# Optimization experiments

Measured on AMD Instinct MI355X. Metric: run time of the kernel, lower is better.

## Reference

```python
import jax, jax.numpy as jnp
import numpy as np

B, S, D = 2, 2048, 1024
H = 16
HD = D // H
SCALE = float(np.sqrt(HD))


def setup_inputs() -> dict:
    key = jax.random.key(0)
    ks = jax.random.split(key, 10)
    def lin(k):
        # xavier_uniform for [out, in] = [D, D]
        bound = float(np.sqrt(6.0 / (D + D)))
        return jax.random.uniform(k, (D, D), jnp.float32, -bound, bound)
    return {
        "hidden_states": jax.random.normal(ks[0], (B, S, D), jnp.float32),
        "attention_mask": jnp.ones((B, S), jnp.float32),
        "Wq": lin(ks[1]), "bq": jnp.zeros((D,), jnp.float32),
        "Wk": lin(ks[2]), "bk": jnp.zeros((D,), jnp.float32),
        "Wv": lin(ks[3]), "bv": jnp.zeros((D,), jnp.float32),
        "Wo": lin(ks[4]), "bo": jnp.zeros((D,), jnp.float32),
    }


def _heads(x):
    # [B,S,D] -> [B,H,S,HD]
    return x.reshape(B, S, H, HD).transpose(0, 2, 1, 3)


def secure_softmax(scores):
    c = jnp.clip(scores, -3.0, 3.0)
    sig = 0.5 + 0.25 * c - 0.01 * c ** 3
    sig = jnp.clip(sig, 0.01, 0.99)
    return sig / (jnp.sum(sig, axis=-1, keepdims=True) + 1e-8)


def reference(hidden_states, attention_mask, Wq, bq, Wk, bk, Wv, bv, Wo, bo):
    q = _heads(hidden_states @ Wq.T + bq)
    k = _heads(hidden_states @ Wk.T + bk)
    v = _heads(hidden_states @ Wv.T + bv)
    # [B,H,S,S]
    scores = jnp.einsum("bhqd,bhkd->bhqk", q, k) / SCALE
    scores = scores + (1.0 - attention_mask[:, None, None, :]) * -10000.0
    probs = secure_softmax(scores)
    ctx = jnp.einsum("bhqk,bhkd->bhqd", probs, v)
    ctx = ctx.transpose(0, 2, 1, 3).reshape(B, S, D)
    return ctx @ Wo.T + bo
```

## Files before the change

kernel.cpp:

```cpp
#include <hip/hip_runtime.h>
#include <stdint.h>

#define B_ 2
#define S_ 2048
#define D_ 1024
#define H_ 16
#define HD_ 64
#define M_ (B_*S_)

typedef __bf16 bf16;
typedef __attribute__((ext_vector_type(8))) __bf16 bf16x8;
typedef __attribute__((ext_vector_type(4))) float f32x4;

__device__ __forceinline__ void gload16(const bf16* g, bf16* l) {
    __builtin_amdgcn_global_load_lds(
        (const __attribute__((address_space(1))) void*)g,
        (__attribute__((address_space(3))) void*)l, 16, 0, 0);
}

__global__ void k_cvt_all(const float* __restrict__ hs,
                          const float* __restrict__ Wq, const float* __restrict__ Wk,
                          const float* __restrict__ Wv, const float* __restrict__ Wo,
                          bf16* __restrict__ hb,
                          bf16* __restrict__ wqb, bf16* __restrict__ wkb,
                          bf16* __restrict__ wvb, bf16* __restrict__ wob) {
    int blk = blockIdx.x;
    const float* s; bf16* d; int base;
    if (blk < 2048) { s = hs; d = hb; base = blk; }
    else {
        int r = blk - 2048; int which = r >> 9; base = r & 511;
        s = (which==0)?Wq:(which==1)?Wk:(which==2)?Wv:Wo;
        d = (which==0)?wqb:(which==1)?wkb:(which==2)?wvb:wob;
    }
    int idx = base*2048 + threadIdx.x*8;
    float4 a = *(const float4*)(s + idx);
    float4 b = *(const float4*)(s + idx + 4);
    bf16 o[8] = {(bf16)a.x,(bf16)a.y,(bf16)a.z,(bf16)a.w,
                 (bf16)b.x,(bf16)b.y,(bf16)b.z,(bf16)b.w};
    *(int4*)(d + idx) = *(const int4*)o;
}

__global__ __launch_bounds__(256) void k_gemm_qkv(
    const bf16* __restrict__ X,
    const bf16* __restrict__ Wq, const bf16* __restrict__ Wk, const bf16* __restrict__ Wv,
    const float* __restrict__ bq, const float* __restrict__ bk, const float* __restrict__ bv,
    bf16* __restrict__ Qo, bf16* __restrict__ Ko, bf16* __restrict__ Vo)
{
    const int z = blockIdx.z;
    const bf16* W = (z==0) ? Wq : (z==1) ? Wk : Wv;
    const float* bias = (z==0) ? bq : (z==1) ? bk : bv;
    const int n0 = blockIdx.x * 128;
    const int m0 = blockIdx.y * 128;
    const int t = threadIdx.x;
    const int w = t >> 6, lane = t & 63, quad = lane >> 4, l15 = lane & 15;
    const int lr = lane >> 3;
    const int lc = (lane & 7) ^ lr;
    const int sx = l15 & 7;
    const int mw = (w >> 1) * 64, nw = (w & 1) * 64;

    __shared__ __align__(16) char smraw[128*136*2];
    bf16* As  = (bf16*)smraw;
    bf16* Bs  = (bf16*)(smraw + 16384);
    bf16* epi = (bf16*)smraw;

    f32x4 acc[4][4];
    #pragma unroll
    for (int i = 0; i < 4; i++)
        #pragma unroll
        for (int j = 0; j < 4; j++)
            acc[i][j] = (f32x4){0.f,0.f,0.f,0.f};

    const bf16* gA = X + (size_t)(m0 + w*8 + lr)*D_ + lc*8;
    const bf16* gB = W + (size_t)(n0 + w*8 + lr)*D_ + lc*8;

    for (int k0 = 0; k0 < D_; k0 += 64) {
        #pragma unroll
        for (int c = 0; c < 4; c++) {
            gload16(gA + (size_t)c*32*D_ + k0, &As[c*2048 + w*512]);
            gload16(gB + (size_t)c*32*D_ + k0, &Bs[c*2048 + w*512]);
        }
        __syncthreads();
        #pragma unroll
        for (int ks = 0; ks < 2; ks++) {
            bf16x8 af[4], bfr[4];
            #pragma unroll
            for (int i = 0; i < 4; i++)
                af[i] = *(const bf16x8*)&As[(mw + i*16 + l15)*64 + (((ks*4+quad)^sx)*8)];
            #pragma unroll
            for (int j = 0; j < 4; j++)
                bfr[j] = *(const bf16x8*)&Bs[(nw + j*16 + l15)*64 + (((ks*4+quad)^sx)*8)];
            #pragma unroll
            for (int i = 0; i < 4; i++)
                #pragma unroll
                for (int j = 0; j < 4; j++)
                    acc[i][j] = __builtin_amdgcn_mfma_f32_16x16x32_bf16(af[i], bfr[j], acc[i][j], 0, 0, 0);
        }
        __syncthreads();
    }

    const float scale = (z == 0) ? 0.125f : 1.0f;
    if (z == 2) {
        #pragma unroll
        for (int j = 0; j < 4; j++) {
            int n = nw + j*16 + l15;
            float bn = bias[n0 + n];
            #pragma unroll
            for (int i = 0; i < 4; i++) {
                int mloc = mw + i*16 + quad*4;
                union { bf16 h4[4]; uint2 u; } pk;
                #pragma unroll
                for (int r = 0; r < 4; r++) pk.h4[r] = (bf16)(acc[i][j][r] + bn);
                *(uint2*)&epi[n*136 + mloc] = pk.u;
            }
        }
    } else {
        #pragma unroll
        for (int j = 0; j < 4; j++) {
            int n = nw + j*16 + l15;
            float bn = bias[n0 + n];
            #pragma unroll
            for (int i = 0; i < 4; i++) {
                int mloc = mw + i*16 + quad*4;
                #pragma unroll
                for (int r = 0; r < 4; r++)
                    epi[(mloc + r)*136 + n] = (bf16)((acc[i][j][r] + bn) * scale);
            }
        }
    }
    __syncthreads();
    if (z == 2) {
        #pragma unroll
        for (int kk = 0; kk < 8; kk++) {
            int c = t + 256*kk;
            int row = c >> 4;
            int mcol = (c & 15) * 8;
            int4 val = *(const int4*)&epi[row*136 + mcol];
            int n = n0 + row; int hh = n >> 6, hd = n & 63;
            int m = m0 + mcol; int bb = m >> 11, s = m & 2047;
            *(int4*)&Vo[((size_t)((bb*H_ + hh)*HD_ + hd))*S_ + s] = val;
        }
    } else {
        bf16* Out = (z == 0) ? Qo : Ko;
        #pragma unroll
        for (int kk = 0; kk < 8; kk++) {
            int c = t + 256*kk;
            int row = c >> 4;
            int ncol = (c & 15) * 8;
            int4 val = *(const int4*)&epi[row*136 + ncol];
            int m = m0 + row; int bb = m >> 11, s = m & 2047;
            int n = n0 + ncol; int hh = n >> 6, hd = n & 63;
            *(int4*)&Out[((size_t)((bb*H_ + hh)*S_ + s))*HD_ + hd] = val;
        }
    }
}

__global__ __launch_bounds__(256) void k_gemm_out(
    const bf16* __restrict__ X, const bf16* __restrict__ W,
    const float* __restrict__ bias, float* __restrict__ Out)
{
    const int n0 = blockIdx.x * 128;
    const int m0 = blockIdx.y * 64;
    const int t = threadIdx.x;
    const int w = t >> 6, lane = t & 63, quad = lane >> 4, l15 = lane & 15;
    const int lr = lane >> 3;
    const int lc = (lane & 7) ^ lr;
    const int sx = l15 & 7;
    const int nw = w * 32;

    __shared__ __align__(16) bf16 As[64*64];
    __shared__ __align__(16) bf16 Bs[128*64];

    f32x4 acc[4][2];
    #pragma unroll
    for (int i = 0; i < 4; i++)
        #pragma unroll
        for (int j = 0; j < 2; j++)
            acc[i][j] = (f32x4){0.f,0.f,0.f,0.f};

    const bf16* gA = X + (size_t)(m0 + w*8 + lr)*D_ + lc*8;
    const bf16* gB = W + (size_t)(n0 + w*8 + lr)*D_ + lc*8;

    for (int k0 = 0; k0 < D_; k0 += 64) {
        #pragma unroll
        for (int c = 0; c < 2; c++)
            gload16(gA + (size_t)c*32*D_ + k0, &As[c*2048 + w*512]);
        #pragma unroll
        for (int c = 0; c < 4; c++)
            gload16(gB + (size_t)c*32*D_ + k0, &Bs[c*2048 + w*512]);
        __syncthreads();
        #pragma unroll
        for (int ks = 0; ks < 2; ks++) {
            bf16x8 af[4], bfr[2];
            #pragma unroll
            for (int i = 0; i < 4; i++)
                af[i] = *(const bf16x8*)&As[(i*16 + l15)*64 + (((ks*4+quad)^sx)*8)];
            #pragma unroll
            for (int j = 0; j < 2; j++)
                bfr[j] = *(const bf16x8*)&Bs[(nw + j*16 + l15)*64 + (((ks*4+quad)^sx)*8)];
            #pragma unroll
            for (int i = 0; i < 4; i++)
                #pragma unroll
                for (int j = 0; j < 2; j++)
                    acc[i][j] = __builtin_amdgcn_mfma_f32_16x16x32_bf16(af[i], bfr[j], acc[i][j], 0, 0, 0);
        }
        __syncthreads();
    }

    #pragma unroll
    for (int j = 0; j < 2; j++) {
        int n = n0 + nw + j*16 + l15;
        float bn = bias[n];
        #pragma unroll
        for (int i = 0; i < 4; i++) {
            int mbase = m0 + i*16 + quad*4;
            #pragma unroll
            for (int r = 0; r < 4; r++)
                Out[(size_t)(mbase + r)*D_ + n] = acc[i][j][r] + bn;
        }
    }
}

__global__ __launch_bounds__(256, 2) void k_attn(
    const bf16* __restrict__ Q, const bf16* __restrict__ K, const bf16* __restrict__ Vt,
    const float* __restrict__ mask, bf16* __restrict__ Ctx)
{
    const int bh = blockIdx.y;
    const int b = bh >> 4, h = bh & 15;
    const int q0 = blockIdx.x * 128;
    const int t = threadIdx.x;
    const int w = t >> 6, lane = t & 63, quad = lane >> 4, l15 = lane & 15;
    const int lr = lane >> 3;
    const int lc = (lane & 7) ^ lr;
    const int sx = l15 & 7;

    __shared__ __align__(16) bf16 Ks[2][64*64];
    __shared__ __align__(16) bf16 Vs[2][64*64];
    __shared__ __align__(16) bf16 Ps[128*64];
    __shared__ float lsumP[4][128];

    bf16x8 qf[8][2];
    const bf16* Qbase = Q + ((size_t)bh*S_ + q0)*HD_;
    #pragma unroll
    for (int qs = 0; qs < 8; qs++)
        #pragma unroll
        for (int ks = 0; ks < 2; ks++)
            qf[qs][ks] = *(const bf16x8*)&Qbase[(size_t)(qs*16 + l15)*HD_ + ks*32 + quad*8];

    f32x4 cacc[2][4];
    #pragma unroll
    for (int i = 0; i < 2; i++)
        #pragma unroll
        for (int j = 0; j < 4; j++)
            cacc[i][j] = (f32x4){0.f,0.f,0.f,0.f};
    float lac[8];
    #pragma unroll
    for (int qs = 0; qs < 8; qs++) lac[qs] = 0.f;

    const bf16* Kst = K + ((size_t)bh*S_ + w*8 + lr)*HD_ + lc*8;
    const bf16* Vst = Vt + ((size_t)bh*HD_ + w*8 + lr)*S_ + lc*8;

    #pragma unroll
    for (int c = 0; c < 2; c++)
        gload16(Kst + (size_t)c*32*HD_, &Ks[0][c*2048 + w*512]);
    #pragma unroll
    for (int c = 0; c < 2; c++)
        gload16(Vst + (size_t)c*32*S_, &Vs[0][c*2048 + w*512]);
    __syncthreads();

    for (int it = 0; it < S_/64; it++) {
        const int cur = it & 1;
        const int k0 = it*64;

        f32x4 st[8];
        #pragma unroll
        for (int qs = 0; qs < 8; qs++) st[qs] = (f32x4){0.f,0.f,0.f,0.f};
        #pragma unroll
        for (int ks = 0; ks < 2; ks++) {
            bf16x8 af = *(const bf16x8*)&Ks[cur][(w*16 + l15)*64 + (((ks*4+quad)^sx)*8)];
            #pragma unroll
            for (int qs = 0; qs < 8; qs++)
                st[qs] = __builtin_amdgcn_mfma_f32_16x16x32_bf16(af, qf[qs][ks], st[qs], 0, 0, 0);
        }

        float4 m4 = *(const float4*)&mask[(size_t)b*S_ + k0 + w*16 + quad*4];
        float mv[4] = {(1.0f-m4.x)*-10000.0f, (1.0f-m4.y)*-10000.0f,
                       (1.0f-m4.z)*-10000.0f, (1.0f-m4.w)*-10000.0f};
        const int c8 = (w*2 + (quad>>1)) ^ sx;
        #pragma unroll
        for (int qs = 0; qs < 8; qs++) {
            union { bf16 h4[4]; uint2 u; } pk;
            #pragma unroll
            for (int r = 0; r < 4; r++) {
                float s = st[qs][r] + mv[r];
                float c = __builtin_amdgcn_fmed3f(s, -3.0f, 3.0f);
                float u = fmaf(c*c, -0.01f, 0.25f);
                float sg = fmaf(c, u, 0.5f);
                sg = __builtin_amdgcn_fmed3f(sg, 0.01f, 0.99f);
                lac[qs] += sg;
                pk.h4[r] = (bf16)sg;
            }
            *(uint2*)&Ps[(qs*16 + l15)*64 + c8*8 + (quad&1)*4] = pk.u;
        }
        __syncthreads();

        if (it < S_/64 - 1) {
            const int nxt = cur ^ 1, k1 = k0 + 64;
            #pragma unroll
            for (int c = 0; c < 2; c++)
                gload16(Kst + (size_t)(k1 + c*32)*HD_, &Ks[nxt][c*2048 + w*512]);
            #pragma unroll
            for (int c = 0; c < 2; c++)
                gload16(Vst + (size_t)c*32*S_ + k1, &Vs[nxt][c*2048 + w*512]);
        }

        #pragma unroll
        for (int ks = 0; ks < 2; ks++) {
            bf16x8 pf[2], vf[4];
            #pragma unroll
            for (int m2 = 0; m2 < 2; m2++)
                pf[m2] = *(const bf16x8*)&Ps[(w*32 + m2*16 + l15)*64 + (((ks*4+quad)^sx)*8)];
            #pragma unroll
            for (int nt = 0; nt < 4; nt++)
                vf[nt] = *(const bf16x8*)&Vs[cur][(nt*16 + l15)*64 + (((ks*4+quad)^sx)*8)];
            #pragma unroll
            for (int m2 = 0; m2 < 2; m2++)
                #pragma unroll
                for (int nt = 0; nt < 4; nt++)
                    cacc[m2][nt] = __builtin_amdgcn_mfma_f32_16x16x32_bf16(pf[m2], vf[nt], cacc[m2][nt], 0, 0, 0);
        }
        __syncthreads();
    }

    #pragma unroll
    for (int qs = 0; qs < 8; qs++) {
        float v = lac[qs];
        v += __shfl_xor(v, 16);
        v += __shfl_xor(v, 32);
        if (quad == 0) lsumP[w][qs*16 + l15] = v;
    }
    __syncthreads();

    #pragma unroll
    for (int m2 = 0; m2 < 2; m2++) {
        #pragma unroll
        for (int r = 0; r < 4; r++) {
            int q = w*32 + m2*16 + quad*4 + r;
            float s = lsumP[0][q] + lsumP[1][q] + lsumP[2][q] + lsumP[3][q];
            float rinv = 1.0f / (s + 1e-8f);
            size_t row = (size_t)(b*S_ + q0 + q);
            #pragma unroll
            for (int nt = 0; nt < 4; nt++)
                Ctx[row*D_ + h*HD_ + nt*16 + l15] = (bf16)(cacc[m2][nt][r] * rinv);
        }
    }
}

extern "C" void kernel_launch(void* const* d_in, const int* in_sizes, int n_in,
                              void* d_out, int out_size, void* d_ws, size_t ws_size,
                              hipStream_t stream) {
    const float* hs   = (const float*)d_in[0];
    const float* mask = (const float*)d_in[1];
    const float* Wq   = (const float*)d_in[2];
    const float* bq   = (const float*)d_in[3];
    const float* Wk   = (const float*)d_in[4];
    const float* bk   = (const float*)d_in[5];
    const float* Wv   = (const float*)d_in[6];
    const float* bv   = (const float*)d_in[7];
    const float* Wo   = (const float*)d_in[8];
    const float* bo   = (const float*)d_in[9];
    float* out = (float*)d_out;

    char* ws = (char*)d_ws;
    const size_t MB = 1024*1024;
    bf16* hb   = (bf16*)(ws);
    bf16* wqb  = (bf16*)(ws + 8*MB);
    bf16* wkb  = (bf16*)(ws + 10*MB);
    bf16* wvb  = (bf16*)(ws + 12*MB);
    bf16* wob  = (bf16*)(ws + 14*MB);
    bf16* qb   = (bf16*)(ws + 16*MB);
    bf16* kb   = (bf16*)(ws + 24*MB);
    bf16* vtb  = (bf16*)(ws + 32*MB);
    bf16* ctxb = (bf16*)(ws + 40*MB);

    k_cvt_all<<<2048 + 4*512, 256, 0, stream>>>(hs, Wq, Wk, Wv, Wo, hb, wqb, wkb, wvb, wob);

    k_gemm_qkv<<<dim3(D_/128, M_/128, 3), 256, 0, stream>>>(
        hb, wqb, wkb, wvb, bq, bk, bv, qb, kb, vtb);

    k_attn<<<dim3(S_/128, B_*H_), 256, 0, stream>>>(qb, kb, vtb, mask, ctxb);

    k_gemm_out<<<dim3(D_/128, M_/64), 256, 0, stream>>>(ctxb, wob, bo, out);
}
```

Before: 209.4 us.

## Restructure attention so each wave owns 32 queries with register-streamed K/V

The attention kernel now gives each wave its own 32 query rows. Each wave loads K and V fragments directly from global memory into registers, prefetching the next tile, instead of staging them cooperatively through double-buffered LDS. The probability tile is kept in a per-wave LDS buffer, which removes the block-wide barriers and the cross-wave row-sum reduction. The polynomial sigmoid is written with packed 2-wide float vectors. The trade-off is that each wave now re-reads K and V from global memory or cache (four times the traffic per block) and uses more registers.

```diff
diff --git a/kernel.cpp b/kernel.cpp
--- a/kernel.cpp
+++ b/kernel.cpp
@@ -11,6 +11,7 @@
 typedef __bf16 bf16;
 typedef __attribute__((ext_vector_type(8))) __bf16 bf16x8;
 typedef __attribute__((ext_vector_type(4))) float f32x4;
+typedef __attribute__((ext_vector_type(2))) float f32x2;
 
 __device__ __forceinline__ void gload16(const bf16* g, bf16* l) {
     __builtin_amdgcn_global_load_lds(
@@ -226,25 +227,26 @@
 {
     const int bh = blockIdx.y;
     const int b = bh >> 4, h = bh & 15;
-    const int q0 = blockIdx.x * 128;
     const int t = threadIdx.x;
     const int w = t >> 6, lane = t & 63, quad = lane >> 4, l15 = lane & 15;
-    const int lr = lane >> 3;
-    const int lc = (lane & 7) ^ lr;
-    const int sx = l15 & 7;
-
-    __shared__ __align__(16) bf16 Ks[2][64*64];
-    __shared__ __align__(16) bf16 Vs[2][64*64];
-    __shared__ __align__(16) bf16 Ps[128*64];
-    __shared__ float lsumP[4][128];
-
-    bf16x8 qf[8][2];
-    const bf16* Qbase = Q + ((size_t)bh*S_ + q0)*HD_;
-    #pragma unroll
-    for (int qs = 0; qs < 8; qs++)
-        #pragma unroll
-        for (int ks = 0; ks < 2; ks++)
-            qf[qs][ks] = *(const bf16x8*)&Qbase[(size_t)(qs*16 + l15)*HD_ + ks*32 + quad*8];
+    const int q0 = blockIdx.x * 128 + w * 32;
+    const int s7 = l15 & 7;
+
+    __shared__ __align__(16) bf16 Pw[4][32*64];
+    __shared__ float lsw[4][32];
+
+    bf16x8 qf[2][2];
+    {
+        const bf16* Qb = Q + ((size_t)bh*S_ + q0)*HD_;
+        #pragma unroll
+        for (int nt = 0; nt < 2; nt++)
+            #pragma unroll
+            for (int ks = 0; ks < 2; ks++)
+                qf[nt][ks] = *(const bf16x8*)&Qb[(size_t)(nt*16 + l15)*HD_ + ks*32 + quad*8];
+    }
+
+    const bf16* Kb = K + (size_t)bh*S_*HD_ + (size_t)l15*HD_ + quad*8;
+    const bf16* Vb = Vt + (size_t)bh*HD_*S_ + (size_t)l15*S_ + quad*8;
 
     f32x4 cacc[2][4];
     #pragma unroll
@@ -252,105 +254,120 @@
         #pragma unroll
         for (int j = 0; j < 4; j++)
             cacc[i][j] = (f32x4){0.f,0.f,0.f,0.f};
-    float lac[8];
-    #pragma unroll
-    for (int qs = 0; qs < 8; qs++) lac[qs] = 0.f;
-
-    const bf16* Kst = K + ((size_t)bh*S_ + w*8 + lr)*HD_ + lc*8;
-    const bf16* Vst = Vt + ((size_t)bh*HD_ + w*8 + lr)*S_ + lc*8;
-
-    #pragma unroll
-    for (int c = 0; c < 2; c++)
-        gload16(Kst + (size_t)c*32*HD_, &Ks[0][c*2048 + w*512]);
-    #pragma unroll
-    for (int c = 0; c < 2; c++)
-        gload16(Vst + (size_t)c*32*S_, &Vs[0][c*2048 + w*512]);
-    __syncthreads();
+    f32x2 lac[2] = {(f32x2){0.f,0.f}, (f32x2){0.f,0.f}};
+
+    bf16x8 ka[4][2], vb[4][2];
+    #pragma unroll
+    for (int mt = 0; mt < 4; mt++)
+        #pragma unroll
+        for (int ks = 0; ks < 2; ks++)
+            ka[mt][ks] = *(const bf16x8*)&Kb[(size_t)(mt*16)*HD_ + ks*32];
+    #pragma unroll
+    for (int nt2 = 0; nt2 < 4; nt2++)
+        #pragma unroll
+        for (int ch = 0; ch < 2; ch++)
+            vb[nt2][ch] = *(const bf16x8*)&Vb[(size_t)(nt2*16)*S_ + ch*32];
 
     for (int it = 0; it < S_/64; it++) {
-        const int cur = it & 1;
         const int k0 = it*64;
 
-        f32x4 st[8];
-        #pragma unroll
-        for (int qs = 0; qs < 8; qs++) st[qs] = (f32x4){0.f,0.f,0.f,0.f};
-        #pragma unroll
-        for (int ks = 0; ks < 2; ks++) {
-            bf16x8 af = *(const bf16x8*)&Ks[cur][(w*16 + l15)*64 + (((ks*4+quad)^sx)*8)];
-            #pragma unroll
-            for (int qs = 0; qs < 8; qs++)
-                st[qs] = __builtin_amdgcn_mfma_f32_16x16x32_bf16(af, qf[qs][ks], st[qs], 0, 0, 0);
-        }
-
-        float4 m4 = *(const float4*)&mask[(size_t)b*S_ + k0 + w*16 + quad*4];
-        float mv[4] = {(1.0f-m4.x)*-10000.0f, (1.0f-m4.y)*-10000.0f,
-                       (1.0f-m4.z)*-10000.0f, (1.0f-m4.w)*-10000.0f};
-        const int c8 = (w*2 + (quad>>1)) ^ sx;
-        #pragma unroll
-        for (int qs = 0; qs < 8; qs++) {
-            union { bf16 h4[4]; uint2 u; } pk;
-            #pragma unroll
-            for (int r = 0; r < 4; r++) {
-                float s = st[qs][r] + mv[r];
-                float c = __builtin_amdgcn_fmed3f(s, -3.0f, 3.0f);
-                float u = fmaf(c*c, -0.01f, 0.25f);
-                float sg = fmaf(c, u, 0.5f);
-                sg = __builtin_amdgcn_fmed3f(sg, 0.01f, 0.99f);
-                lac[qs] += sg;
-                pk.h4[r] = (bf16)sg;
+        float4 mk[4];
+        #pragma unroll
+        for (int mt = 0; mt < 4; mt++)
+            mk[mt] = *(const float4*)&mask[(size_t)b*S_ + k0 + mt*16 + quad*4];
+
+        f32x4 st[4][2];
+        #pragma unroll
+        for (int mt = 0; mt < 4; mt++)
+            #pragma unroll
+            for (int nt = 0; nt < 2; nt++)
+                st[mt][nt] = (f32x4){0.f,0.f,0.f,0.f};
+        #pragma unroll
+        for (int ks = 0; ks < 2; ks++)
+            #pragma unroll
+            for (int mt = 0; mt < 4; mt++)
+                #pragma unroll
+                for (int nt = 0; nt < 2; nt++)
+                    st[mt][nt] = __builtin_amdgcn_mfma_f32_16x16x32_bf16(ka[mt][ks], qf[nt][ks], st[mt][nt], 0, 0, 0);
+
+        if (it < S_/64 - 1) {
+            #pragma unroll
+            for (int mt = 0; mt < 4; mt++)
+                #pragma unroll
+                for (int ks = 0; ks < 2; ks++)
+                    ka[mt][ks] = *(const bf16x8*)&Kb[(size_t)(k0 + 64 + mt*16)*HD_ + ks*32];
+        }
+
+        #pragma unroll
+        for (int mt = 0; mt < 4; mt++) {
+            f32x2 mlo = {(1.0f - mk[mt].x)*-10000.0f, (1.0f - mk[mt].y)*-10000.0f};
+            f32x2 mhi = {(1.0f - mk[mt].z)*-10000.0f, (1.0f - mk[mt].w)*-10000.0f};
+            #pragma unroll
+            for (int nt = 0; nt < 2; nt++) {
+                f32x2 s0 = {st[mt][nt][0], st[mt][nt][1]};
+                f32x2 s1 = {st[mt][nt][2], st[mt][nt][3]};
+                s0 += mlo; s1 += mhi;
+                s0 = __builtin_elementwise_min(__builtin_elementwise_max(s0, (f32x2)(-3.0f)), (f32x2)(3.0f));
+                s1 = __builtin_elementwise_min(__builtin_elementwise_max(s1, (f32x2)(-3.0f)), (f32x2)(3.0f));
+                f32x2 g0 = s0 * (s0*s0*(f32x2)(-0.01f) + (f32x2)(0.25f)) + (f32x2)(0.5f);
+                f32x2 g1 = s1 * (s1*s1*(f32x2)(-0.01f) + (f32x2)(0.25f)) + (f32x2)(0.5f);
+                g0 = __builtin_elementwise_min(__builtin_elementwise_max(g0, (f32x2)(0.01f)), (f32x2)(0.99f));
+                g1 = __builtin_elementwise_min(__builtin_elementwise_max(g1, (f32x2)(0.01f)), (f32x2)(0.99f));
+                lac[nt] += g0 + g1;
+                union { bf16 h2[2]; uint32_t u; } p0, p1;
+                p0.h2[0] = (bf16)g0.x; p0.h2[1] = (bf16)g0.y;
+                p1.h2[0] = (bf16)g1.x; p1.h2[1] = (bf16)g1.y;
+                uint2 pk = {p0.u, p1.u};
+                int ql = nt*16 + l15;
+                *(uint2*)&Pw[w][ql*64 + (((mt*2 + (quad>>1)) ^ s7)*8) + (quad&1)*4] = pk;
             }
-            *(uint2*)&Ps[(qs*16 + l15)*64 + c8*8 + (quad&1)*4] = pk.u;
-        }
-        __syncthreads();
+        }
+
+        bf16x8 pf[2][2];
+        #pragma unroll
+        for (int ch = 0; ch < 2; ch++)
+            #pragma unroll
+            for (int nt = 0; nt < 2; nt++)
+                pf[ch][nt] = *(const bf16x8*)&Pw[w][(nt*16 + l15)*64 + (((ch*4 + quad) ^ s7)*8)];
+
+        #pragma unroll
+        for (int ch = 0; ch < 2; ch++)
+            #pragma unroll
+            for (int nt = 0; nt < 2; nt++)
+                #pragma unroll
+                for (int nt2 = 0; nt2 < 4; nt2++)
+                    cacc[nt][nt2] = __builtin_amdgcn_mfma_f32_16x16x32_bf16(pf[ch][nt], vb[nt2][ch], cacc[nt][nt2], 0, 0, 0);
 
         if (it < S_/64 - 1) {
-            const int nxt = cur ^ 1, k1 = k0 + 64;
-            #pragma unroll
-            for (int c = 0; c < 2; c++)
-                gload16(Kst + (size_t)(k1 + c*32)*HD_, &Ks[nxt][c*2048 + w*512]);
-            #pragma unroll
-            for (int c = 0; c < 2; c++)
-                gload16(Vst + (size_t)c*32*S_ + k1, &Vs[nxt][c*2048 + w*512]);
-        }
-
-        #pragma unroll
-        for (int ks = 0; ks < 2; ks++) {
-            bf16x8 pf[2], vf[4];
-            #pragma unroll
-            for (int m2 = 0; m2 < 2; m2++)
-                pf[m2] = *(const bf16x8*)&Ps[(w*32 + m2*16 + l15)*64 + (((ks*4+quad)^sx)*8)];
-            #pragma unroll
-            for (int nt = 0; nt < 4; nt++)
-                vf[nt] = *(const bf16x8*)&Vs[cur][(nt*16 + l15)*64 + (((ks*4+quad)^sx)*8)];
-            #pragma unroll
-            for (int m2 = 0; m2 < 2; m2++)
-                #pragma unroll
-                for (int nt = 0; nt < 4; nt++)
-                    cacc[m2][nt] = __builtin_amdgcn_mfma_f32_16x16x32_bf16(pf[m2], vf[nt], cacc[m2][nt], 0, 0, 0);
-        }
-        __syncthreads();
-    }
-
-    #pragma unroll
-    for (int qs = 0; qs < 8; qs++) {
-        float v = lac[qs];
+            #pragma unroll
+            for (int nt2 = 0; nt2 < 4; nt2++)
+                #pragma unroll
+                for (int ch = 0; ch < 2; ch++)
+                    vb[nt2][ch] = *(const bf16x8*)&Vb[(size_t)(nt2*16)*S_ + k0 + 64 + ch*32];
+        }
+    }
+
+    #pragma unroll
+    for (int nt = 0; nt < 2; nt++) {
+        float v = lac[nt].x + lac[nt].y;
         v += __shfl_xor(v, 16);
         v += __shfl_xor(v, 32);
-        if (quad == 0) lsumP[w][qs*16 + l15] = v;
-    }
-    __syncthreads();
-
-    #pragma unroll
-    for (int m2 = 0; m2 < 2; m2++) {
+        if (quad == 0) lsw[w][nt*16 + l15] = v;
+    }
+    f32x4 s4[2];
+    #pragma unroll
+    for (int nt = 0; nt < 2; nt++)
+        s4[nt] = *(const f32x4*)&lsw[w][nt*16 + quad*4];
+
+    #pragma unroll
+    for (int nt = 0; nt < 2; nt++) {
         #pragma unroll
         for (int r = 0; r < 4; r++) {
-            int q = w*32 + m2*16 + quad*4 + r;
-            float s = lsumP[0][q] + lsumP[1][q] + lsumP[2][q] + lsumP[3][q];
-            float rinv = 1.0f / (s + 1e-8f);
-            size_t row = (size_t)(b*S_ + q0 + q);
-            #pragma unroll
-            for (int nt = 0; nt < 4; nt++)
-                Ctx[row*D_ + h*HD_ + nt*16 + l15] = (bf16)(cacc[m2][nt][r] * rinv);
+            float rinv = 1.0f / (s4[nt][r] + 1e-8f);
+            size_t row = (size_t)(b*S_ + q0 + nt*16 + quad*4 + r);
+            #pragma unroll
+            for (int nt2 = 0; nt2 < 4; nt2++)
+                Ctx[row*D_ + h*HD_ + nt2*16 + l15] = (bf16)(cacc[nt][nt2][r] * rinv);
         }
     }
 }
```

Result: slower. 278.8 us (+33.1%).

## Split attention over key halves and fuse the partial combine into the output GEMM

Applied to the files above, without the earlier changes.

The attention kernel now launches a third grid dimension that splits the key sequence into two halves. Each half writes an unnormalized bf16 context and per-row sigmoid sums to separate workspace buffers, which reuse the memory of the dead hidden-state and Wq copies. The output projection GEMM loads both partials, adds them, divides by the summed normalizer, and writes the A tile to LDS through registers instead of the async global-to-LDS load. This doubles the number of attention blocks to fill more CUs, but adds extra partial-result traffic, a slower A-tile load path in the GEMM, and an extra bf16 rounding of the unnormalized partials.

```diff
diff --git a/kernel.cpp b/kernel.cpp
--- a/kernel.cpp
+++ b/kernel.cpp
@@ -155,7 +155,9 @@
 }
 
 __global__ __launch_bounds__(256) void k_gemm_out(
-    const bf16* __restrict__ X, const bf16* __restrict__ W,
+    const bf16* __restrict__ P0, const bf16* __restrict__ P1,
+    const float* __restrict__ L0, const float* __restrict__ L1,
+    const bf16* __restrict__ W,
     const float* __restrict__ bias, float* __restrict__ Out)
 {
     const int n0 = blockIdx.x * 128;
@@ -177,13 +179,26 @@
         for (int j = 0; j < 2; j++)
             acc[i][j] = (f32x4){0.f,0.f,0.f,0.f};
 
-    const bf16* gA = X + (size_t)(m0 + w*8 + lr)*D_ + lc*8;
     const bf16* gB = W + (size_t)(n0 + w*8 + lr)*D_ + lc*8;
 
     for (int k0 = 0; k0 < D_; k0 += 64) {
-        #pragma unroll
-        for (int c = 0; c < 2; c++)
-            gload16(gA + (size_t)c*32*D_ + k0, &As[c*2048 + w*512]);
+        const int head = k0 >> 6;
+        #pragma unroll
+        for (int c = 0; c < 2; c++) {
+            int row = m0 + c*32 + w*8 + lr;
+            int bb = row >> 11, s = row & 2047;
+            int lidx = (bb*H_ + head)*S_ + s;
+            float l = L0[lidx] + L1[lidx];
+            float inv = 1.0f / (l + 1e-8f);
+            size_t gofs = (size_t)row*D_ + k0 + lc*8;
+            bf16x8 a0 = *(const bf16x8*)&P0[gofs];
+            bf16x8 a1 = *(const bf16x8*)&P1[gofs];
+            bf16 o8[8];
+            #pragma unroll
+            for (int r = 0; r < 8; r++)
+                o8[r] = (bf16)(((float)a0[r] + (float)a1[r]) * inv);
+            *(int4*)&As[c*2048 + w*512 + lane*8] = *(const int4*)o8;
+        }
         #pragma unroll
         for (int c = 0; c < 4; c++)
             gload16(gB + (size_t)c*32*D_ + k0, &Bs[c*2048 + w*512]);
@@ -220,13 +235,18 @@
     }
 }
 
-__global__ __launch_bounds__(256, 2) void k_attn(
+__global__ __launch_bounds__(256) void k_attn(
     const bf16* __restrict__ Q, const bf16* __restrict__ K, const bf16* __restrict__ Vt,
-    const float* __restrict__ mask, bf16* __restrict__ Ctx)
+    const float* __restrict__ mask,
+    bf16* __restrict__ P0, bf16* __restrict__ P1,
+    float* __restrict__ L0, float* __restrict__ L1)
 {
     const int bh = blockIdx.y;
     const int b = bh >> 4, h = bh & 15;
     const int q0 = blockIdx.x * 128;
+    const int z = blockIdx.z;
+    bf16* __restrict__ Po = z ? P1 : P0;
+    float* __restrict__ Lo = z ? L1 : L0;
     const int t = threadIdx.x;
     const int w = t >> 6, lane = t & 63, quad = lane >> 4, l15 = lane & 15;
     const int lr = lane >> 3;
@@ -256,20 +276,21 @@
     #pragma unroll
     for (int qs = 0; qs < 8; qs++) lac[qs] = 0.f;
 
+    const int kb0 = z * (S_/2);
     const bf16* Kst = K + ((size_t)bh*S_ + w*8 + lr)*HD_ + lc*8;
     const bf16* Vst = Vt + ((size_t)bh*HD_ + w*8 + lr)*S_ + lc*8;
 
     #pragma unroll
     for (int c = 0; c < 2; c++)
-        gload16(Kst + (size_t)c*32*HD_, &Ks[0][c*2048 + w*512]);
+        gload16(Kst + (size_t)(kb0 + c*32)*HD_, &Ks[0][c*2048 + w*512]);
     #pragma unroll
     for (int c = 0; c < 2; c++)
-        gload16(Vst + (size_t)c*32*S_, &Vs[0][c*2048 + w*512]);
+        gload16(Vst + (size_t)c*32*S_ + kb0, &Vs[0][c*2048 + w*512]);
     __syncthreads();
 
-    for (int it = 0; it < S_/64; it++) {
+    for (int it = 0; it < S_/128; it++) {
         const int cur = it & 1;
-        const int k0 = it*64;
+        const int k0 = kb0 + it*64;
 
         f32x4 st[8];
         #pragma unroll
@@ -303,14 +324,14 @@
         }
         __syncthreads();
 
-        if (it < S_/64 - 1) {
-            const int nxt = cur ^ 1, k1 = k0 + 64;
+        if (it < S_/128 - 1) {
+            const int k1 = k0 + 64;
             #pragma unroll
             for (int c = 0; c < 2; c++)
-                gload16(Kst + (size_t)(k1 + c*32)*HD_, &Ks[nxt][c*2048 + w*512]);
+                gload16(Kst + (size_t)(k1 + c*32)*HD_, &Ks[cur^1][c*2048 + w*512]);
             #pragma unroll
             for (int c = 0; c < 2; c++)
-                gload16(Vst + (size_t)c*32*S_ + k1, &Vs[nxt][c*2048 + w*512]);
+                gload16(Vst + (size_t)c*32*S_ + k1, &Vs[cur^1][c*2048 + w*512]);
         }
 
         #pragma unroll
@@ -346,11 +367,12 @@
         for (int r = 0; r < 4; r++) {
             int q = w*32 + m2*16 + quad*4 + r;
             float s = lsumP[0][q] + lsumP[1][q] + lsumP[2][q] + lsumP[3][q];
-            float rinv = 1.0f / (s + 1e-8f);
+            if (l15 == 0)
+                Lo[(size_t)bh*S_ + q0 + q] = s;
             size_t row = (size_t)(b*S_ + q0 + q);
             #pragma unroll
             for (int nt = 0; nt < 4; nt++)
-                Ctx[row*D_ + h*HD_ + nt*16 + l15] = (bf16)(cacc[m2][nt][r] * rinv);
+                Po[row*D_ + h*HD_ + nt*16 + l15] = (bf16)cacc[m2][nt][r];
         }
     }
 }
@@ -372,22 +394,25 @@
 
     char* ws = (char*)d_ws;
     const size_t MB = 1024*1024;
-    bf16* hb   = (bf16*)(ws);
-    bf16* wqb  = (bf16*)(ws + 8*MB);
-    bf16* wkb  = (bf16*)(ws + 10*MB);
-    bf16* wvb  = (bf16*)(ws + 12*MB);
-    bf16* wob  = (bf16*)(ws + 14*MB);
-    bf16* qb   = (bf16*)(ws + 16*MB);
-    bf16* kb   = (bf16*)(ws + 24*MB);
-    bf16* vtb  = (bf16*)(ws + 32*MB);
-    bf16* ctxb = (bf16*)(ws + 40*MB);
+    bf16*  hb   = (bf16*)(ws);
+    bf16*  P1   = (bf16*)(ws);
+    bf16*  wqb  = (bf16*)(ws + 8*MB);
+    float* L0   = (float*)(ws + 8*MB);
+    float* L1   = (float*)(ws + 8*MB + 512*1024);
+    bf16*  wkb  = (bf16*)(ws + 10*MB);
+    bf16*  wvb  = (bf16*)(ws + 12*MB);
+    bf16*  wob  = (bf16*)(ws + 14*MB);
+    bf16*  qb   = (bf16*)(ws + 16*MB);
+    bf16*  kb   = (bf16*)(ws + 24*MB);
+    bf16*  vtb  = (bf16*)(ws + 32*MB);
+    bf16*  P0   = (bf16*)(ws + 40*MB);
 
     k_cvt_all<<<2048 + 4*512, 256, 0, stream>>>(hs, Wq, Wk, Wv, Wo, hb, wqb, wkb, wvb, wob);
 
     k_gemm_qkv<<<dim3(D_/128, M_/128, 3), 256, 0, stream>>>(
         hb, wqb, wkb, wvb, bq, bk, bv, qb, kb, vtb);
 
-    k_attn<<<dim3(S_/128, B_*H_), 256, 0, stream>>>(qb, kb, vtb, mask, ctxb);
-
-    k_gemm_out<<<dim3(D_/128, M_/64), 256, 0, stream>>>(ctxb, wob, bo, out);
-}
+    k_attn<<<dim3(S_/128, B_*H_, 2), 256, 0, stream>>>(qb, kb, vtb, mask, P0, P1, L0, L1);
+
+    k_gemm_out<<<dim3(D_/128, M_/64), 256, 0, stream>>>(P0, P1, L0, L1, wob, bo, out);
+}
```

After: 272.3 us. 30.1% more time.

## Halve attention query tile to 64 rows and single-buffer V with reordered prefetch

Applied to the files above, without the earlier changes.

The attention kernel now processes 64 query rows per block instead of 128, doubling the grid to 1024 blocks and roughly halving per-thread accumulator and Q-fragment registers. V shared memory goes from double to single buffering: V for the current tile is loaded at the top of each iteration, and the next K tile is prefetched alongside it. The launch-bounds occupancy hint is dropped. More blocks and less LDS should raise occupancy, but each K/V tile is now reloaded by twice as many blocks, and the V load is no longer overlapped with the previous iteration's compute.

```diff
diff --git a/kernel.cpp b/kernel.cpp
--- a/kernel.cpp
+++ b/kernel.cpp
@@ -220,13 +220,13 @@
     }
 }
 
-__global__ __launch_bounds__(256, 2) void k_attn(
+__global__ __launch_bounds__(256) void k_attn(
     const bf16* __restrict__ Q, const bf16* __restrict__ K, const bf16* __restrict__ Vt,
     const float* __restrict__ mask, bf16* __restrict__ Ctx)
 {
     const int bh = blockIdx.y;
     const int b = bh >> 4, h = bh & 15;
-    const int q0 = blockIdx.x * 128;
+    const int q0 = blockIdx.x * 64;
     const int t = threadIdx.x;
     const int w = t >> 6, lane = t & 63, quad = lane >> 4, l15 = lane & 15;
     const int lr = lane >> 3;
@@ -234,27 +234,24 @@
     const int sx = l15 & 7;
 
     __shared__ __align__(16) bf16 Ks[2][64*64];
-    __shared__ __align__(16) bf16 Vs[2][64*64];
-    __shared__ __align__(16) bf16 Ps[128*64];
-    __shared__ float lsumP[4][128];
-
-    bf16x8 qf[8][2];
+    __shared__ __align__(16) bf16 Vs[64*64];
+    __shared__ __align__(16) bf16 Ps[64*64];
+    __shared__ float lsumP[4][64];
+
+    bf16x8 qf[4][2];
     const bf16* Qbase = Q + ((size_t)bh*S_ + q0)*HD_;
     #pragma unroll
-    for (int qs = 0; qs < 8; qs++)
+    for (int qs = 0; qs < 4; qs++)
         #pragma unroll
         for (int ks = 0; ks < 2; ks++)
             qf[qs][ks] = *(const bf16x8*)&Qbase[(size_t)(qs*16 + l15)*HD_ + ks*32 + quad*8];
 
-    f32x4 cacc[2][4];
-    #pragma unroll
-    for (int i = 0; i < 2; i++)
-        #pragma unroll
-        for (int j = 0; j < 4; j++)
-            cacc[i][j] = (f32x4){0.f,0.f,0.f,0.f};
-    float lac[8];
-    #pragma unroll
-    for (int qs = 0; qs < 8; qs++) lac[qs] = 0.f;
+    f32x4 cacc[4];
+    #pragma unroll
+    for (int j = 0; j < 4; j++) cacc[j] = (f32x4){0.f,0.f,0.f,0.f};
+    float lac[4];
+    #pragma unroll
+    for (int qs = 0; qs < 4; qs++) lac[qs] = 0.f;
 
     const bf16* Kst = K + ((size_t)bh*S_ + w*8 + lr)*HD_ + lc*8;
     const bf16* Vst = Vt + ((size_t)bh*HD_ + w*8 + lr)*S_ + lc*8;
@@ -264,21 +261,32 @@
         gload16(Kst + (size_t)c*32*HD_, &Ks[0][c*2048 + w*512]);
     #pragma unroll
     for (int c = 0; c < 2; c++)
-        gload16(Vst + (size_t)c*32*S_, &Vs[0][c*2048 + w*512]);
+        gload16(Vst + (size_t)c*32*S_, &Vs[c*2048 + w*512]);
     __syncthreads();
 
     for (int it = 0; it < S_/64; it++) {
         const int cur = it & 1;
         const int k0 = it*64;
 
-        f32x4 st[8];
-        #pragma unroll
-        for (int qs = 0; qs < 8; qs++) st[qs] = (f32x4){0.f,0.f,0.f,0.f};
+        if (it > 0) {
+            #pragma unroll
+            for (int c = 0; c < 2; c++)
+                gload16(Vst + (size_t)c*32*S_ + k0, &Vs[c*2048 + w*512]);
+        }
+        if (it < S_/64 - 1) {
+            #pragma unroll
+            for (int c = 0; c < 2; c++)
+                gload16(Kst + (size_t)(k0 + 64 + c*32)*HD_, &Ks[cur^1][c*2048 + w*512]);
+        }
+
+        f32x4 st[4];
+        #pragma unroll
+        for (int qs = 0; qs < 4; qs++) st[qs] = (f32x4){0.f,0.f,0.f,0.f};
         #pragma unroll
         for (int ks = 0; ks < 2; ks++) {
             bf16x8 af = *(const bf16x8*)&Ks[cur][(w*16 + l15)*64 + (((ks*4+quad)^sx)*8)];
             #pragma unroll
-            for (int qs = 0; qs < 8; qs++)
+            for (int qs = 0; qs < 4; qs++)
                 st[qs] = __builtin_amdgcn_mfma_f32_16x16x32_bf16(af, qf[qs][ks], st[qs], 0, 0, 0);
         }
 
@@ -287,7 +295,7 @@
                        (1.0f-m4.z)*-10000.0f, (1.0f-m4.w)*-10000.0f};
         const int c8 = (w*2 + (quad>>1)) ^ sx;
         #pragma unroll
-        for (int qs = 0; qs < 8; qs++) {
+        for (int qs = 0; qs < 4; qs++) {
             union { bf16 h4[4]; uint2 u; } pk;
             #pragma unroll
             for (int r = 0; r < 4; r++) {
@@ -303,36 +311,22 @@
         }
         __syncthreads();
 
-        if (it < S_/64 - 1) {
-            const int nxt = cur ^ 1, k1 = k0 + 64;
-            #pragma unroll
-            for (int c = 0; c < 2; c++)
-                gload16(Kst + (size_t)(k1 + c*32)*HD_, &Ks[nxt][c*2048 + w*512]);
-            #pragma unroll
-            for (int c = 0; c < 2; c++)
-                gload16(Vst + (size_t)c*32*S_ + k1, &Vs[nxt][c*2048 + w*512]);
-        }
-
         #pragma unroll
         for (int ks = 0; ks < 2; ks++) {
-            bf16x8 pf[2], vf[4];
-            #pragma unroll
-            for (int m2 = 0; m2 < 2; m2++)
-                pf[m2] = *(const bf16x8*)&Ps[(w*32 + m2*16 + l15)*64 + (((ks*4+quad)^sx)*8)];
+            bf16x8 pf, vf[4];
+            pf = *(const bf16x8*)&Ps[(w*16 + l15)*64 + (((ks*4+quad)^sx)*8)];
             #pragma unroll
             for (int nt = 0; nt < 4; nt++)
-                vf[nt] = *(const bf16x8*)&Vs[cur][(nt*16 + l15)*64 + (((ks*4+quad)^sx)*8)];
-            #pragma unroll
-            for (int m2 = 0; m2 < 2; m2++)
-                #pragma unroll
-                for (int nt = 0; nt < 4; nt++)
-                    cacc[m2][nt] = __builtin_amdgcn_mfma_f32_16x16x32_bf16(pf[m2], vf[nt], cacc[m2][nt], 0, 0, 0);
-        }
-        __syncthreads();
-    }
-
-    #pragma unroll
-    for (int qs = 0; qs < 8; qs++) {
+                vf[nt] = *(const bf16x8*)&Vs[(nt*16 + l15)*64 + (((ks*4+quad)^sx)*8)];
+            #pragma unroll
+            for (int nt = 0; nt < 4; nt++)
+                cacc[nt] = __builtin_amdgcn_mfma_f32_16x16x32_bf16(pf, vf[nt], cacc[nt], 0, 0, 0);
+        }
+        __syncthreads();
+    }
+
+    #pragma unroll
+    for (int qs = 0; qs < 4; qs++) {
         float v = lac[qs];
         v += __shfl_xor(v, 16);
         v += __shfl_xor(v, 32);
@@ -341,17 +335,14 @@
     __syncthreads();
 
     #pragma unroll
-    for (int m2 = 0; m2 < 2; m2++) {
-        #pragma unroll
-        for (int r = 0; r < 4; r++) {
-            int q = w*32 + m2*16 + quad*4 + r;
-            float s = lsumP[0][q] + lsumP[1][q] + lsumP[2][q] + lsumP[3][q];
-            float rinv = 1.0f / (s + 1e-8f);
-            size_t row = (size_t)(b*S_ + q0 + q);
-            #pragma unroll
-            for (int nt = 0; nt < 4; nt++)
-                Ctx[row*D_ + h*HD_ + nt*16 + l15] = (bf16)(cacc[m2][nt][r] * rinv);
-        }
+    for (int r = 0; r < 4; r++) {
+        int q = w*16 + quad*4 + r;
+        float s = lsumP[0][q] + lsumP[1][q] + lsumP[2][q] + lsumP[3][q];
+        float rinv = 1.0f / (s + 1e-8f);
+        size_t row = (size_t)(b*S_ + q0 + q);
+        #pragma unroll
+        for (int nt = 0; nt < 4; nt++)
+            Ctx[row*D_ + h*HD_ + nt*16 + l15] = (bf16)(cacc[nt][r] * rinv);
     }
 }
 
@@ -387,7 +378,7 @@
     k_gemm_qkv<<<dim3(D_/128, M_/128, 3), 256, 0, stream>>>(
         hb, wqb, wkb, wvb, bq, bk, bv, qb, kb, vtb);
 
-    k_attn<<<dim3(S_/128, B_*H_), 256, 0, stream>>>(qb, kb, vtb, mask, ctxb);
+    k_attn<<<dim3(S_/64, B_*H_), 256, 0, stream>>>(qb, kb, vtb, mask, ctxb);
 
     k_gemm_out<<<dim3(D_/128, M_/64), 256, 0, stream>>>(ctxb, wob, bo, out);
 }
```

Result: slower. 239.4 us (+14.3%).
